# Kernel tuning notes

Measured on AMD Instinct MI355X. Metric: run time of the kernel, lower is better.

## Reference

```python
import jax, jax.numpy as jnp
import numpy as np

B, N_PER, P_PER = 64, 64, 2016   # graphs, nodes/graph, pairs/graph (C(64,2))
IN_DIM, HID, OUT = 64, 128, 10
EDGE_P = 0.125


def _build_graph_structures():
    """Integer preprocessing replicating build_2sets_from_embeddings's
    combinatorics (pairs, iso_type source, triangle-based 2-set edges)."""
    rng = np.random.default_rng(0)
    n, b = N_PER, B
    A = rng.random((b, n, n)) < EDGE_P
    A = np.triu(A, 1)
    A = A | A.transpose(0, 2, 1)                      # symmetric, no self loops
    gs, us, vs = np.nonzero(A)                        # directed edges, both dirs
    edge_index = np.stack([gs * n + us, gs * n + vs]).astype(np.int64)
    batch = np.repeat(np.arange(b), n).astype(np.int64)
    iu, iv = np.triu_indices(n, 1)                    # local pair (u<v) lists
    pidx = np.full((n, n), -1, np.int64)
    pidx[iu, iv] = np.arange(P_PER)
    pidx[iv, iu] = np.arange(P_PER)                   # symmetric lookup = sorted()
    pair_u = (np.arange(b)[:, None] * n + iu[None, :]).ravel().astype(np.int64)
    pair_v = (np.arange(b)[:, None] * n + iv[None, :]).ravel().astype(np.int64)
    iso_type = A[:, iu, iv].astype(np.float32).ravel()[:, None]  # [B*P_PER,1]
    # 2-set edges: pair (u,v) -> sorted(v,w) and sorted(u,w) for every common
    # neighbor w of u and v (matches _build_2set_edges exactly)
    common = A[:, iu, :] & A[:, iv, :]                # (B, P_PER, n)
    g2, ps, ws = np.nonzero(common)
    u, v = iu[ps], iv[ps]
    d1 = pidx[v, ws]
    d2 = pidx[u, ws]
    src = np.concatenate([g2 * P_PER + ps, g2 * P_PER + ps])
    dst = np.concatenate([g2 * P_PER + d1, g2 * P_PER + d2])
    two_edges = np.stack([src, dst]).astype(np.int64)
    two_batch = np.repeat(np.arange(b), P_PER).astype(np.int64)
    return edge_index, batch, pair_u, pair_v, iso_type, two_edges, two_batch


def setup_inputs() -> dict:
    ei, batch, pu, pv, iso, te, tb = _build_graph_structures()
    key = jax.random.key(0)
    ks = jax.random.split(key, 16)
    w = lambda k, i, o: jax.random.normal(k, (i, o), jnp.float32) / np.float32(np.sqrt(i))
    two_in = 2 * HID + 1
    return {
        "x": jax.random.normal(ks[0], (B * N_PER, IN_DIM), jnp.float32),
        "g1_W1_0": w(ks[1], IN_DIM, HID), "g1_W2_0": w(ks[2], IN_DIM, HID),
        "g1_W1_1": w(ks[3], HID, HID),    "g1_W2_1": w(ks[4], HID, HID),
        "g1_W1_2": w(ks[5], HID, HID),    "g1_W2_2": w(ks[6], HID, HID),
        "k_W1_0": w(ks[7], two_in, HID),  "k_W2_0": w(ks[8], two_in, HID),
        "k_W1_1": w(ks[9], HID, HID),     "k_W2_1": w(ks[10], HID, HID),
        "c_W0": w(ks[11], 2 * HID, HID),  "c_b0": jnp.zeros((HID,), jnp.float32),
        "c_W1": w(ks[12], HID, OUT),      "c_b1": jnp.zeros((OUT,), jnp.float32),
        "iso_type": jnp.asarray(iso),
        "edge_index": jnp.asarray(ei), "batch": jnp.asarray(batch),
        "pair_u": jnp.asarray(pu), "pair_v": jnp.asarray(pv),
        "two_edges": jnp.asarray(te), "two_batch": jnp.asarray(tb),
    }


def _mp_layer(h, ei, W1, W2):
    # relu( h @ W1 + scatter_add_{dst}( h[src] @ W2 ) )  -- OneGNNLayer / KSetLayer
    msg = h[ei[0]] @ W2
    agg = jax.ops.segment_sum(msg, ei[1], num_segments=h.shape[0])
    return jax.nn.relu(h @ W1 + agg)


def reference(x, g1_W1_0, g1_W2_0, g1_W1_1, g1_W2_1, g1_W1_2, g1_W2_2,
              k_W1_0, k_W2_0, k_W1_1, k_W2_1,
              c_W0, c_b0, c_W1, c_b1,
              iso_type, edge_index, batch, pair_u, pair_v, two_edges, two_batch):
    h = _mp_layer(x, edge_index, g1_W1_0, g1_W2_0)
    h = _mp_layer(h, edge_index, g1_W1_1, g1_W2_1)
    h = _mp_layer(h, edge_index, g1_W1_2, g1_W2_2)
    graph_emb_1 = jax.ops.segment_sum(h, batch, num_segments=B)
    # 2-set features: [h_u, h_v, iso_type]  -> [P, 2H+1]
    two_x = jnp.concatenate([h[pair_u], h[pair_v], iso_type], axis=1)
    h2 = _mp_layer(two_x, two_edges, k_W1_0, k_W2_0)
    h2 = _mp_layer(h2, two_edges, k_W1_1, k_W2_1)
    graph_emb_2 = jax.ops.segment_sum(h2, two_batch, num_segments=B)
    combined = jnp.concatenate([graph_emb_1, graph_emb_2], axis=1)
    hc = jax.nn.relu(combined @ c_W0 + c_b0)   # Dropout(p=0.5) inactive in eval
    return hc @ c_W1 + c_b1
```

## Files before the change

kernel.cpp:

```cpp
#include <hip/hip_runtime.h>
#include <hip/hip_bf16.h>


typedef short s16x8 __attribute__((ext_vector_type(8)));
typedef float f32x4 __attribute__((ext_vector_type(4)));

__device__ __forceinline__ unsigned short f2bf(float f) {
  union { float f; unsigned u; } x; x.f = f;
  unsigned r = (x.u + 0x7fffu + ((x.u >> 16) & 1u)) >> 16;
  return (unsigned short)r;
}
__device__ __forceinline__ float bf2f(unsigned short h) {
  union { unsigned u; float f; } x; x.u = ((unsigned)h) << 16;
  return x.f;
}
__device__ __forceinline__ float4 ldbf4(const unsigned short* p) {
  ushort4 q = *(const ushort4*)p;
  return make_float4(bf2f(q.x), bf2f(q.y), bf2f(q.z), bf2f(q.w));
}
__device__ __forceinline__ void stbf4(unsigned short* p, float4 v) {
  ushort4 q;
  q.x = f2bf(v.x); q.y = f2bf(v.y); q.z = f2bf(v.z); q.w = f2bf(v.w);
  *(ushort4*)p = q;
}
__device__ __forceinline__ float4 ld4(const float* p) { return *(const float4*)p; }

template<int KCS, int ASTR>
__device__ __forceinline__ void mfma_dual_lds(
    const unsigned short* A, const unsigned short* Wfrag,
    f32x4 (&accA)[8], f32x4 (&accB)[8])
{
  const int lane = threadIdx.x & 63;
  const int wv = threadIdx.x >> 6;
  const int row = wv * 16 + (lane & 15);
  const int k0 = (lane >> 4) << 3;
  const unsigned short* ap = A + row * ASTR + k0;
  const unsigned short* wp = Wfrag + (size_t)lane * 8;
#pragma unroll
  for (int i = 0; i < 8; ++i) { accA[i] = (f32x4)0.f; accB[i] = (f32x4)0.f; }
#pragma unroll
  for (int kc = 0; kc < KCS; ++kc) {
    s16x8 af = *(const s16x8*)(ap + kc * 32);
#pragma unroll
    for (int nt = 0; nt < 8; ++nt) {
      s16x8 b0 = *(const s16x8*)(wp + ((size_t)((nt)*KCS + kc) << 9));
      s16x8 b1 = *(const s16x8*)(wp + ((size_t)((8 + nt) * KCS + kc) << 9));
      accA[nt] = __builtin_amdgcn_mfma_f32_16x16x32_bf16(af, b0, accA[nt], 0, 0, 0);
      accB[nt] = __builtin_amdgcn_mfma_f32_16x16x32_bf16(af, b1, accB[nt], 0, 0, 0);
    }
  }
}

template<int KCS, int ASTR>
__device__ __forceinline__ void mfma_dual_lds16(
    const unsigned short* A, const unsigned short* Wfrag,
    f32x4 (&accA)[2], f32x4 (&accB)[2])
{
  const int lane = threadIdx.x & 63;
  const int w16 = threadIdx.x >> 6;
  const int rw = w16 & 3, ch = w16 >> 2;
  const int row = rw * 16 + (lane & 15);
  const int k0 = (lane >> 4) << 3;
  const unsigned short* ap = A + row * ASTR + k0;
  const unsigned short* wp = Wfrag + (size_t)lane * 8;
  accA[0] = (f32x4)0.f; accA[1] = (f32x4)0.f;
  accB[0] = (f32x4)0.f; accB[1] = (f32x4)0.f;
  __builtin_amdgcn_s_setprio(1);
#pragma unroll
  for (int kc = 0; kc < KCS; ++kc) {
    s16x8 af = *(const s16x8*)(ap + kc * 32);
#pragma unroll
    for (int n2 = 0; n2 < 2; ++n2) {
      int nt = ch * 2 + n2;
      s16x8 b0 = *(const s16x8*)(wp + ((size_t)(nt * KCS + kc) << 9));
      s16x8 b1 = *(const s16x8*)(wp + ((size_t)((8 + nt) * KCS + kc) << 9));
      accA[n2] = __builtin_amdgcn_mfma_f32_16x16x32_bf16(af, b0, accA[n2], 0, 0, 0);
      accB[n2] = __builtin_amdgcn_mfma_f32_16x16x32_bf16(af, b1, accB[n2], 0, 0, 0);
    }
  }
  __builtin_amdgcn_s_setprio(0);
}

__device__ __forceinline__ void epi_lds16(const f32x4 (&accA)[2], const f32x4 (&accB)[2],
    unsigned short (*preS)[136], unsigned short (*msgS)[136])
{
  const int lane = threadIdx.x & 63;
  const int w16 = threadIdx.x >> 6;
  const int rw = w16 & 3, ch = w16 >> 2;
  const int col = lane & 15;
  const int r0 = rw * 16 + ((lane >> 4) << 2);
  __syncthreads();
#pragma unroll
  for (int n2 = 0; n2 < 2; ++n2) {
    int nt = ch * 2 + n2;
#pragma unroll
    for (int r = 0; r < 4; ++r) {
      preS[r0 + r][nt * 16 + col] = f2bf(accA[n2][r]);
      msgS[r0 + r][nt * 16 + col] = f2bf(accB[n2][r]);
    }
  }
  __syncthreads();
}

__device__ __forceinline__ void epi_global(const f32x4 (&accA)[8], const f32x4 (&accB)[8],
    unsigned short (*sOut)[136], unsigned short* Ca, unsigned short* Cb, long tile)
{
  const int tid = threadIdx.x;
  const int lane = tid & 63;
  const int wv = tid >> 6;
  const int col = lane & 15;
  const int r0 = wv * 16 + ((lane >> 4) << 2);
  const long rowBase = tile * 64;
#pragma unroll
  for (int sel = 0; sel < 2; ++sel) {
    __syncthreads();
#pragma unroll
    for (int nt = 0; nt < 8; ++nt) {
#pragma unroll
      for (int r = 0; r < 4; ++r)
        sOut[r0 + r][nt * 16 + col] = f2bf(sel ? accB[nt][r] : accA[nt][r]);
    }
    __syncthreads();
    unsigned short* C = sel ? Cb : Ca;
#pragma unroll
    for (int i = 0; i < 4; ++i) {
      int fi = tid + i * 256;
      int row = fi >> 4;
      int c8 = fi & 15;
      *(uint4*)(C + (rowBase + row) * 128 + c8 * 8) = *(uint4*)&sOut[row][c8 * 8];
    }
  }
}

struct NArgs {
  const float* x;
  const int* ei;
  const int* gstart;
  const unsigned short *Wf0, *Wf1, *Wf2;
  unsigned short* Hn;
  float* ge1;
  int E1;
};

__global__ __launch_bounds__(1024) void node_stage(NArgs a)
{
  __shared__ __align__(16) unsigned short hS[64][136];
  __shared__ __align__(16) unsigned short preS[64][136];
  __shared__ __align__(16) unsigned short msgS[64][136];
  __shared__ int ldeg[64], lcur[64], loff[65];
  __shared__ unsigned short ledge[1024];
  __shared__ float sge[128];

  const int b = blockIdx.x;
  const int t = threadIdx.x;
  const int base = b * 64;

  const int es = a.gstart[b], ee = a.gstart[b + 1];
  if (t < 64) ldeg[t] = 0;
  if (t < 128) sge[t] = 0.f;
  __syncthreads();
  for (int i = es + t; i < ee; i += 1024)
    atomicAdd(&ldeg[a.ei[a.E1 + i] - base], 1);
  __syncthreads();
  if (t < 64) {
    int v = ldeg[t], s = v;
#pragma unroll
    for (int d = 1; d < 64; d <<= 1) {
      int o = __shfl_up(s, d, 64);
      if (t >= d) s += o;
    }
    loff[t] = s - v;
    lcur[t] = s - v;
    if (t == 63) loff[64] = s;
  }
  unsigned short* xs = &preS[0][0];
  for (int i = t; i < 64 * 64; i += 1024) {
    int r = i >> 6, c = i & 63;
    xs[r * 72 + c] = f2bf(a.x[(size_t)(base + r) * 64 + c]);
  }
  __syncthreads();
  for (int i = es + t; i < ee; i += 1024) {
    int s = a.ei[i] - base, d = a.ei[a.E1 + i] - base;
    int pos = atomicAdd(&lcur[d], 1);
    ledge[pos] = (unsigned short)s;
  }
  __syncthreads();

  f32x4 accA[2], accB[2];
  const int grp = t >> 5, f = (t & 31) * 4;

  mfma_dual_lds16<2, 72>(xs, a.Wf0, accA, accB);
  epi_lds16(accA, accB, preS, msgS);
  for (int r = grp; r < 64; r += 32) {
    float4 acc = ldbf4(&preS[r][f]);
    int j1 = loff[r + 1];
    for (int j = loff[r]; j < j1; ++j) {
      float4 m = ldbf4(&msgS[ledge[j]][f]);
      acc.x += m.x; acc.y += m.y; acc.z += m.z; acc.w += m.w;
    }
    stbf4(&hS[r][f], make_float4(fmaxf(acc.x, 0.f), fmaxf(acc.y, 0.f),
                                 fmaxf(acc.z, 0.f), fmaxf(acc.w, 0.f)));
  }
  __syncthreads();

  mfma_dual_lds16<4, 136>(&hS[0][0], a.Wf1, accA, accB);
  epi_lds16(accA, accB, preS, msgS);
  for (int r = grp; r < 64; r += 32) {
    float4 acc = ldbf4(&preS[r][f]);
    int j1 = loff[r + 1];
    for (int j = loff[r]; j < j1; ++j) {
      float4 m = ldbf4(&msgS[ledge[j]][f]);
      acc.x += m.x; acc.y += m.y; acc.z += m.z; acc.w += m.w;
    }
    stbf4(&hS[r][f], make_float4(fmaxf(acc.x, 0.f), fmaxf(acc.y, 0.f),
                                 fmaxf(acc.z, 0.f), fmaxf(acc.w, 0.f)));
  }
  __syncthreads();

  mfma_dual_lds16<4, 136>(&hS[0][0], a.Wf2, accA, accB);
  epi_lds16(accA, accB, preS, msgS);
  {
    float4 g = make_float4(0.f, 0.f, 0.f, 0.f);
    for (int r = grp; r < 64; r += 32) {
      float4 acc = ldbf4(&preS[r][f]);
      int j1 = loff[r + 1];
      for (int j = loff[r]; j < j1; ++j) {
        float4 m = ldbf4(&msgS[ledge[j]][f]);
        acc.x += m.x; acc.y += m.y; acc.z += m.z; acc.w += m.w;
      }
      float4 o = make_float4(fmaxf(acc.x, 0.f), fmaxf(acc.y, 0.f),
                             fmaxf(acc.z, 0.f), fmaxf(acc.w, 0.f));
      stbf4(&hS[r][f], o);
      g.x += o.x; g.y += o.y; g.z += o.z; g.w += o.w;
    }
    atomicAdd(&sge[f + 0], g.x);
    atomicAdd(&sge[f + 1], g.y);
    atomicAdd(&sge[f + 2], g.z);
    atomicAdd(&sge[f + 3], g.w);
  }
  __syncthreads();
  if (t < 128) a.ge1[b * 128 + t] = sge[t];
  {
    int row = t >> 4, c8 = t & 15;
    *(uint4*)(a.Hn + (size_t)(base + row) * 128 + c8 * 8) = *(uint4*)&hS[row][c8 * 8];
  }
}

__global__ __launch_bounds__(256) void hv_gemm(
    const unsigned short* __restrict__ Hn,
    const unsigned short* __restrict__ Wf3, const unsigned short* __restrict__ Wf4,
    unsigned short* __restrict__ HU1, unsigned short* __restrict__ HU2,
    unsigned short* __restrict__ HV1, unsigned short* __restrict__ HV2)
{
  __shared__ __align__(16) unsigned short hS[64][136];
  const int g = blockIdx.x >> 1;
  const int sel = blockIdx.x & 1;
  const int tid = threadIdx.x;
  const unsigned short* src = Hn + (size_t)g * 64 * 128;
#pragma unroll
  for (int i = 0; i < 4; ++i) {
    int fi = tid + i * 256;
    int row = fi >> 4, c8 = fi & 15;
    *(uint4*)&hS[row][c8 * 8] = *(const uint4*)(src + row * 128 + c8 * 8);
  }
  __syncthreads();
  f32x4 accA[8], accB[8];
  mfma_dual_lds<4, 136>(&hS[0][0], sel ? Wf4 : Wf3, accA, accB);
  epi_global(accA, accB, hS, sel ? HV1 : HU1, sel ? HV2 : HU2, g);
}

struct PrepArgs {
  const float* wa[6];
  const float* wb[6];
  unsigned short* Wf[6];
  const int* te; int E2;
  int* degP;
  const int* ei; int E1;
  int* gstart;
  int nCnt;
};

__global__ void prep(PrepArgs p)
{
  int bb = blockIdx.x, t = threadIdx.x;
  if (bb < 88) {
    int gid = bb * 256 + t;
    if (gid < 22528) {
      int pi, local, kcs, kclog;
      if (gid < 2048) { pi = 0; local = gid; kcs = 2; kclog = 1; }
      else { int r = gid - 2048; pi = 1 + (r >> 12); local = r & 4095; kcs = 4; kclog = 2; }
      int lane = local & 63;
      int t1 = local >> 6;
      int kc = t1 & (kcs - 1);
      int t2 = t1 >> kclog;
      int nt = t2 & 7;
      int wsel = t2 >> 3;
      const float* W = wsel ? p.wb[pi] : p.wa[pi];
      int k0 = kc * 32 + ((lane >> 4) << 3);
      int n = nt * 16 + (lane & 15);
      unsigned short tmp[8];
#pragma unroll
      for (int j = 0; j < 8; ++j) tmp[j] = f2bf(W[(size_t)(k0 + j) * 128 + n]);
      *(uint4*)(p.Wf[pi] + (size_t)local * 8) = *(uint4*)tmp;
    }
  } else if (bb < 88 + p.nCnt) {
    int e = (bb - 88) * 256 + t;
    if (e < p.E2) atomicAdd(&p.degP[p.te[p.E2 + e]], 1);
  } else {
    int e = (bb - 88 - p.nCnt) * 256 + t;
    if (e <= p.E1) {
      int ge = (e < p.E1) ? (p.ei[e] >> 6) : 64;
      int gp = (e > 0) ? (p.ei[e - 1] >> 6) : -1;
      for (int g = gp + 1; g <= ge; ++g) p.gstart[g] = e;
    }
  }
}

__global__ __launch_bounds__(256) void scan_reduce(const int* __restrict__ deg,
                                                   int* __restrict__ bsum, int n)
{
  __shared__ int s[256];
  int b = blockIdx.x, t = threadIdx.x;
  int base = b * 1024;
  int v = 0;
#pragma unroll
  for (int i = 0; i < 4; ++i) {
    int idx = base + t + i * 256;
    if (idx < n) v += deg[idx];
  }
  s[t] = v;
  __syncthreads();
  for (int d = 128; d > 0; d >>= 1) {
    if (t < d) s[t] += s[t + d];
    __syncthreads();
  }
  if (t == 0) bsum[b] = s[0];
}

__global__ __launch_bounds__(1024) void scan_partials(int* __restrict__ bsum, int nb)
{
  __shared__ int s[1024];
  int t = threadIdx.x;
  s[t] = (t < nb) ? bsum[t] : 0;
  __syncthreads();
  for (int d = 1; d < 1024; d <<= 1) {
    int v = (t >= d) ? s[t - d] : 0;
    __syncthreads();
    s[t] += v;
    __syncthreads();
  }
  if (t < nb) bsum[t] = (t == 0) ? 0 : s[t - 1];
  if (t == 1023) bsum[nb] = s[1023];
}

__global__ __launch_bounds__(256) void scan_final(const int* __restrict__ deg,
                                                  const int* __restrict__ bsum,
                                                  int* __restrict__ off,
                                                  int* __restrict__ cur, int n, int nb)
{
  __shared__ int s[256];
  int b = blockIdx.x, t = threadIdx.x;
  int base = b * 1024 + t * 4;
  int v0 = 0, v1 = 0, v2 = 0, v3 = 0;
  if (base + 0 < n) v0 = deg[base + 0];
  if (base + 1 < n) v1 = deg[base + 1];
  if (base + 2 < n) v2 = deg[base + 2];
  if (base + 3 < n) v3 = deg[base + 3];
  s[t] = v0 + v1 + v2 + v3;
  __syncthreads();
  for (int d = 1; d < 256; d <<= 1) {
    int v = (t >= d) ? s[t - d] : 0;
    __syncthreads();
    s[t] += v;
    __syncthreads();
  }
  int run = bsum[b] + ((t == 0) ? 0 : s[t - 1]);
  if (base + 0 < n) { off[base + 0] = run; cur[base + 0] = run; run += v0; }
  if (base + 1 < n) { off[base + 1] = run; cur[base + 1] = run; run += v1; }
  if (base + 2 < n) { off[base + 2] = run; cur[base + 2] = run; run += v2; }
  if (base + 3 < n) { off[base + 3] = run; cur[base + 3] = run; run += v3; }
  if (b == 0 && t == 0) off[n] = bsum[nb];
}

__global__ void csr_fill_pair(const int* __restrict__ te, int E2,
                              const int* __restrict__ pu, const int* __restrict__ pv,
                              const float* __restrict__ iso,
                              int* __restrict__ curP, int4* __restrict__ recP)
{
  int e = blockIdx.x * 256 + threadIdx.x;
  if (e >= E2) return;
  int s = te[e], d = te[E2 + e];
  int pos = atomicAdd(&curP[d], 1);
  recP[pos] = make_int4(pu[s], pv[s], __float_as_int(iso[s]), s);
}

__global__ __launch_bounds__(256) void gather_two0_t(
    const unsigned short* __restrict__ HU1, const unsigned short* __restrict__ HV1,
    const unsigned short* __restrict__ HU2, const unsigned short* __restrict__ HV2,
    const float* __restrict__ iso,
    const float* __restrict__ w1iso, const float* __restrict__ w2iso,
    const int* __restrict__ pu, const int* __restrict__ pv,
    const int* __restrict__ off, const int4* __restrict__ rec,
    unsigned short* __restrict__ out)
{
  __shared__ int offS[65];
  __shared__ int puS[64], pvS[64];
  __shared__ float isoS[64];
  __shared__ __align__(16) int4 recS[512];

  const int tid = threadIdx.x;
  int tile = (int)blockIdx.x;
  const int nT = (int)gridDim.x;
  if ((nT & 7) == 0)
    tile = (tile & 7) * (nT >> 3) + (tile >> 3);
  const int p0 = tile * 64;

  if (tid < 65) offS[tid] = off[p0 + tid];
  if (tid < 64) { puS[tid] = pu[p0 + tid]; pvS[tid] = pv[p0 + tid]; isoS[tid] = iso[p0 + tid]; }
  __syncthreads();
  const int e0 = offS[0];
  const int ecnt = offS[64] - e0;
  const bool useS = (ecnt <= 512);
  if (useS)
    for (int j = tid; j < ecnt; j += 256) recS[j] = rec[e0 + j];
  __syncthreads();

  const int grp = tid >> 5;
  const int f = (tid & 31) * 4;
  const float4 wi1 = ld4(w1iso + f);
  const float4 wi2 = ld4(w2iso + f);
  for (int pi = grp; pi < 64; pi += 8) {
    float4 a = ldbf4(HU1 + (size_t)puS[pi] * 128 + f);
    float4 b = ldbf4(HV1 + (size_t)pvS[pi] * 128 + f);
    float is0 = isoS[pi];
    float4 acc;
    acc.x = a.x + b.x + is0 * wi1.x;
    acc.y = a.y + b.y + is0 * wi1.y;
    acc.z = a.z + b.z + is0 * wi1.z;
    acc.w = a.w + b.w + is0 * wi1.w;
    int j = offS[pi], e1 = offS[pi + 1];
    for (; j + 1 < e1; j += 2) {
      int4 r0 = useS ? recS[j - e0] : rec[j];
      int4 r1 = useS ? recS[j + 1 - e0] : rec[j + 1];
      float4 mu0 = ldbf4(HU2 + (size_t)r0.x * 128 + f);
      float4 mv0 = ldbf4(HV2 + (size_t)r0.y * 128 + f);
      float4 mu1 = ldbf4(HU2 + (size_t)r1.x * 128 + f);
      float4 mv1 = ldbf4(HV2 + (size_t)r1.y * 128 + f);
      float i0 = __int_as_float(r0.z), i1 = __int_as_float(r1.z);
      acc.x += mu0.x + mv0.x + i0 * wi2.x + mu1.x + mv1.x + i1 * wi2.x;
      acc.y += mu0.y + mv0.y + i0 * wi2.y + mu1.y + mv1.y + i1 * wi2.y;
      acc.z += mu0.z + mv0.z + i0 * wi2.z + mu1.z + mv1.z + i1 * wi2.z;
      acc.w += mu0.w + mv0.w + i0 * wi2.w + mu1.w + mv1.w + i1 * wi2.w;
    }
    if (j < e1) {
      int4 r0 = useS ? recS[j - e0] : rec[j];
      float4 mu0 = ldbf4(HU2 + (size_t)r0.x * 128 + f);
      float4 mv0 = ldbf4(HV2 + (size_t)r0.y * 128 + f);
      float i0 = __int_as_float(r0.z);
      acc.x += mu0.x + mv0.x + i0 * wi2.x;
      acc.y += mu0.y + mv0.y + i0 * wi2.y;
      acc.z += mu0.z + mv0.z + i0 * wi2.z;
      acc.w += mu0.w + mv0.w + i0 * wi2.w;
    }
    stbf4(out + (size_t)(p0 + pi) * 128 + f,
          make_float4(fmaxf(acc.x, 0.f), fmaxf(acc.y, 0.f),
                      fmaxf(acc.z, 0.f), fmaxf(acc.w, 0.f)));
  }
}

__global__ __launch_bounds__(256) void pair_l1(
    const unsigned short* __restrict__ H2,
    const unsigned short* __restrict__ Wfrag,
    const int* __restrict__ off, const int4* __restrict__ rec,
    float* __restrict__ gep)
{
  __shared__ __align__(16) unsigned short aggS[64][136];
  __shared__ int offS[65];
  __shared__ int recwS[768];
  __shared__ float sge[256];

  const int tid = threadIdx.x;
  int tile = (int)blockIdx.x;
  const int nT = (int)gridDim.x;
  if ((nT & 7) == 0)
    tile = (tile & 7) * (nT >> 3) + (tile >> 3);
  const int r0 = tile * 64;

  if (tid < 65) offS[tid] = off[r0 + tid];
  sge[tid] = 0.f;

  const int lane = tid & 63;
  const int wv = tid >> 6;
  const int arow = wv * 16 + (lane & 15);
  const int k0 = (lane >> 4) << 3;
  const unsigned short* hrow = H2 + (size_t)(r0 + arow) * 128 + k0;
  s16x8 ah[4];
#pragma unroll
  for (int kc = 0; kc < 4; ++kc) ah[kc] = *(const s16x8*)(hrow + kc * 32);

  __syncthreads();
  const int e0 = offS[0];
  const int ecnt = offS[64] - e0;
  const bool useS = (ecnt <= 768);
  if (useS)
    for (int j = tid; j < ecnt; j += 256) recwS[j] = rec[e0 + j].w;
  __syncthreads();

  {
    const int grp = tid >> 5, f = (tid & 31) * 4;
    for (int i = grp; i < 64; i += 8) {
      float4 acc = make_float4(0.f, 0.f, 0.f, 0.f);
      int j = offS[i], e1 = offS[i + 1];
      for (; j + 1 < e1; j += 2) {
        int s0 = useS ? recwS[j - e0] : rec[j].w;
        int s1 = useS ? recwS[j + 1 - e0] : rec[j + 1].w;
        float4 m0 = ldbf4(H2 + (size_t)s0 * 128 + f);
        float4 m1 = ldbf4(H2 + (size_t)s1 * 128 + f);
        acc.x += m0.x + m1.x; acc.y += m0.y + m1.y;
        acc.z += m0.z + m1.z; acc.w += m0.w + m1.w;
      }
      if (j < e1) {
        int s0 = useS ? recwS[j - e0] : rec[j].w;
        float4 m0 = ldbf4(H2 + (size_t)s0 * 128 + f);
        acc.x += m0.x; acc.y += m0.y; acc.z += m0.z; acc.w += m0.w;
      }
      stbf4(&aggS[i][f], acc);
    }
  }
  __syncthreads();

  const unsigned short* gp = &aggS[0][0] + arow * 136 + k0;
  const unsigned short* wp = Wfrag + (size_t)lane * 8;
  f32x4 acc[8];
#pragma unroll
  for (int nt = 0; nt < 8; ++nt) acc[nt] = (f32x4)0.f;
  __builtin_amdgcn_s_setprio(1);
#pragma unroll
  for (int kc = 0; kc < 4; ++kc) {
    s16x8 ag = *(const s16x8*)(gp + kc * 32);
#pragma unroll
    for (int nt = 0; nt < 8; ++nt) {
      s16x8 b0 = *(const s16x8*)(wp + ((size_t)(nt * 4 + kc) << 9));
      s16x8 b1 = *(const s16x8*)(wp + ((size_t)((8 + nt) * 4 + kc) << 9));
      acc[nt] = __builtin_amdgcn_mfma_f32_16x16x32_bf16(ah[kc], b0, acc[nt], 0, 0, 0);
      acc[nt] = __builtin_amdgcn_mfma_f32_16x16x32_bf16(ag, b1, acc[nt], 0, 0, 0);
    }
  }
  __builtin_amdgcn_s_setprio(0);

  const int half = wv >> 1;
  const int col0 = lane & 15;
#pragma unroll
  for (int nt = 0; nt < 8; ++nt) {
    float s = fmaxf(acc[nt][0], 0.f) + fmaxf(acc[nt][1], 0.f)
            + fmaxf(acc[nt][2], 0.f) + fmaxf(acc[nt][3], 0.f);
    atomicAdd(&sge[half * 128 + nt * 16 + col0], s);
  }
  __syncthreads();
  gep[(size_t)tile * 256 + tid] = sge[tid];
}

__global__ void classifier(const float* __restrict__ ge1, const float* __restrict__ gep,
                           const float* __restrict__ W0, const float* __restrict__ b0,
                           const float* __restrict__ W1, const float* __restrict__ b1,
                           float* __restrict__ out)
{
  __shared__ float comb[256];
  __shared__ float hc[128];
  int g = blockIdx.x, t = threadIdx.x;
  comb[t] = ge1[g * 128 + t];
  float s2 = 0.f;
  const float* gpr = gep + (size_t)g * 63 * 128 + t;
  for (int i = 0; i < 63; ++i) s2 += gpr[i * 128];
  comb[t + 128] = s2;
  __syncthreads();
  float s = b0[t];
  for (int k = 0; k < 256; ++k) s += comb[k] * W0[k * 128 + t];
  hc[t] = fmaxf(s, 0.f);
  __syncthreads();
  if (t < 10) {
    float s2o = b1[t];
    for (int k = 0; k < 128; ++k) s2o += hc[k] * W1[k * 10 + t];
    out[g * 10 + t] = s2o;
  }
}

extern "C" void kernel_launch(void* const* d_in, const int* in_sizes, int n_in,
                              void* d_out, int out_size, void* d_ws, size_t ws_size,
                              hipStream_t stream)
{
  (void)n_in; (void)out_size; (void)ws_size;
  const float* x       = (const float*)d_in[0];
  const float* g1_W1_0 = (const float*)d_in[1];
  const float* g1_W2_0 = (const float*)d_in[2];
  const float* g1_W1_1 = (const float*)d_in[3];
  const float* g1_W2_1 = (const float*)d_in[4];
  const float* g1_W1_2 = (const float*)d_in[5];
  const float* g1_W2_2 = (const float*)d_in[6];
  const float* k_W1_0  = (const float*)d_in[7];
  const float* k_W2_0  = (const float*)d_in[8];
  const float* k_W1_1  = (const float*)d_in[9];
  const float* k_W2_1  = (const float*)d_in[10];
  const float* c_W0    = (const float*)d_in[11];
  const float* c_b0    = (const float*)d_in[12];
  const float* c_W1    = (const float*)d_in[13];
  const float* c_b1    = (const float*)d_in[14];
  const float* iso     = (const float*)d_in[15];
  const int*   ei      = (const int*)d_in[16];
  const int*   pu      = (const int*)d_in[18];
  const int*   pv      = (const int*)d_in[19];
  const int*   te      = (const int*)d_in[20];

  const int N  = in_sizes[0] / 64;
  const int E1 = in_sizes[16] / 2;
  const int P  = in_sizes[18];
  const int E2 = in_sizes[20] / 2;
  const int B  = 64;
  const int nTiles = P / 64;

  const size_t NH = (size_t)N * 128;
  const size_t PH = (size_t)P * 128;

  float* ge1 = (float*)d_ws;
  float* gep = ge1 + 8192;
  unsigned short* HU1 = (unsigned short*)(gep + (size_t)2 * nTiles * 128);
  unsigned short* HV1 = HU1 + NH;
  unsigned short* HU2 = HV1 + NH;
  unsigned short* HV2 = HU2 + NH;
  unsigned short* H2   = HV2 + NH;
  unsigned short* Hn   = H2 + PH;
  unsigned short* Wf0  = Hn + NH;
  unsigned short* Wf1  = Wf0 + 16384;
  unsigned short* Wf2  = Wf1 + 32768;
  unsigned short* Wf3  = Wf2 + 32768;
  unsigned short* Wf4  = Wf3 + 32768;
  unsigned short* Wf5  = Wf4 + 32768;

  size_t ipOff = ((size_t)((char*)(Wf5 + 32768) - (char*)d_ws) + 15) & ~(size_t)15;
  int4* recP   = (int4*)((char*)d_ws + ipOff);
  int* degP    = (int*)(recP + E2);
  int* offP    = degP + P;
  int* curP    = offP + P + 1;
  int* bsumP   = curP + P;
  int* gstartN = bsumP + 128;

  const int nbP  = (P + 1023) / 1024;
  const int nCnt = (E2 + 255) / 256;
  const int nBnd = (E1 + 256) / 256;

  hipMemsetAsync(degP, 0, (size_t)P * 4, stream);

  PrepArgs pa;
  pa.wa[0] = g1_W1_0;           pa.wb[0] = g1_W2_0;
  pa.wa[1] = g1_W1_1;           pa.wb[1] = g1_W2_1;
  pa.wa[2] = g1_W1_2;           pa.wb[2] = g1_W2_2;
  pa.wa[3] = k_W1_0;            pa.wb[3] = k_W2_0;
  pa.wa[4] = k_W1_0 + 128*128;  pa.wb[4] = k_W2_0 + 128*128;
  pa.wa[5] = k_W1_1;            pa.wb[5] = k_W2_1;
  pa.Wf[0] = Wf0; pa.Wf[1] = Wf1; pa.Wf[2] = Wf2;
  pa.Wf[3] = Wf3; pa.Wf[4] = Wf4; pa.Wf[5] = Wf5;
  pa.te = te; pa.E2 = E2; pa.degP = degP;
  pa.ei = ei; pa.E1 = E1; pa.gstart = gstartN; pa.nCnt = nCnt;
  prep<<<88 + nCnt + nBnd, 256, 0, stream>>>(pa);

  scan_reduce<<<nbP, 256, 0, stream>>>(degP, bsumP, P);
  scan_partials<<<1, 1024, 0, stream>>>(bsumP, nbP);
  scan_final<<<nbP, 256, 0, stream>>>(degP, bsumP, offP, curP, P, nbP);
  csr_fill_pair<<<nCnt, 256, 0, stream>>>(te, E2, pu, pv, iso, curP, recP);

  NArgs na;
  na.x = x; na.ei = ei; na.gstart = gstartN; na.E1 = E1;
  na.Wf0 = Wf0; na.Wf1 = Wf1; na.Wf2 = Wf2;
  na.Hn = Hn; na.ge1 = ge1;
  node_stage<<<B, 1024, 0, stream>>>(na);

  hv_gemm<<<2 * B, 256, 0, stream>>>(Hn, Wf3, Wf4, HU1, HU2, HV1, HV2);

  gather_two0_t<<<nTiles, 256, 0, stream>>>(HU1, HV1, HU2, HV2, iso,
                                            k_W1_0 + 256 * 128, k_W2_0 + 256 * 128,
                                            pu, pv, offP, recP, H2);

  pair_l1<<<nTiles, 256, 0, stream>>>(H2, Wf5, offP, recP, gep);

  classifier<<<B, 128, 0, stream>>>(ge1, gep, c_W0, c_b0, c_W1, c_b1, (float*)d_out);
}
```

Before: 302.4 us.

## Fuse pair layer-0 gather into pair layer-1 by recomputing neighbor features

Merges the two pair-level kernels into one. Each tile builds its own layer-0 features in shared memory, and it recomputes every neighbor pair's layer-0 row on the fly from the HU/HV tables instead of reading a materialized H2 buffer. This removes the global H2 write and read and one kernel launch. In exchange it adds two-hop gather work proportional to neighbor degree, and the larger shared-memory footprint may lower occupancy.

```diff
diff --git a/kernel.cpp b/kernel.cpp
--- a/kernel.cpp
+++ b/kernel.cpp
@@ -394,19 +394,24 @@
   recP[pos] = make_int4(pu[s], pv[s], __float_as_int(iso[s]), s);
 }
 
-__global__ __launch_bounds__(256) void gather_two0_t(
+__global__ __launch_bounds__(256) void pair_fused(
     const unsigned short* __restrict__ HU1, const unsigned short* __restrict__ HV1,
     const unsigned short* __restrict__ HU2, const unsigned short* __restrict__ HV2,
     const float* __restrict__ iso,
     const float* __restrict__ w1iso, const float* __restrict__ w2iso,
     const int* __restrict__ pu, const int* __restrict__ pv,
     const int* __restrict__ off, const int4* __restrict__ rec,
-    unsigned short* __restrict__ out)
-{
+    const unsigned short* __restrict__ Wfrag,
+    float* __restrict__ gep)
+{
+  __shared__ __align__(16) unsigned short hS[64][136];
+  __shared__ __align__(16) unsigned short aggS[64][136];
   __shared__ int offS[65];
   __shared__ int puS[64], pvS[64];
   __shared__ float isoS[64];
   __shared__ __align__(16) int4 recS[512];
+  __shared__ int so0S[512], so1S[512];
+  __shared__ float sge[256];
 
   const int tid = threadIdx.x;
   int tile = (int)blockIdx.x;
@@ -417,119 +422,92 @@
 
   if (tid < 65) offS[tid] = off[p0 + tid];
   if (tid < 64) { puS[tid] = pu[p0 + tid]; pvS[tid] = pv[p0 + tid]; isoS[tid] = iso[p0 + tid]; }
+  sge[tid] = 0.f;
   __syncthreads();
   const int e0 = offS[0];
   const int ecnt = offS[64] - e0;
   const bool useS = (ecnt <= 512);
-  if (useS)
+  if (useS) {
     for (int j = tid; j < ecnt; j += 256) recS[j] = rec[e0 + j];
+    __syncthreads();
+    for (int j = tid; j < ecnt; j += 256) {
+      int s = recS[j].w;
+      so0S[j] = off[s];
+      so1S[j] = off[s + 1];
+    }
+  }
   __syncthreads();
 
   const int grp = tid >> 5;
   const int f = (tid & 31) * 4;
   const float4 wi1 = ld4(w1iso + f);
   const float4 wi2 = ld4(w2iso + f);
-  for (int pi = grp; pi < 64; pi += 8) {
-    float4 a = ldbf4(HU1 + (size_t)puS[pi] * 128 + f);
-    float4 b = ldbf4(HV1 + (size_t)pvS[pi] * 128 + f);
-    float is0 = isoS[pi];
-    float4 acc;
-    acc.x = a.x + b.x + is0 * wi1.x;
-    acc.y = a.y + b.y + is0 * wi1.y;
-    acc.z = a.z + b.z + is0 * wi1.z;
-    acc.w = a.w + b.w + is0 * wi1.w;
-    int j = offS[pi], e1 = offS[pi + 1];
-    for (; j + 1 < e1; j += 2) {
-      int4 r0 = useS ? recS[j - e0] : rec[j];
-      int4 r1 = useS ? recS[j + 1 - e0] : rec[j + 1];
-      float4 mu0 = ldbf4(HU2 + (size_t)r0.x * 128 + f);
-      float4 mv0 = ldbf4(HV2 + (size_t)r0.y * 128 + f);
-      float4 mu1 = ldbf4(HU2 + (size_t)r1.x * 128 + f);
-      float4 mv1 = ldbf4(HV2 + (size_t)r1.y * 128 + f);
-      float i0 = __int_as_float(r0.z), i1 = __int_as_float(r1.z);
-      acc.x += mu0.x + mv0.x + i0 * wi2.x + mu1.x + mv1.x + i1 * wi2.x;
-      acc.y += mu0.y + mv0.y + i0 * wi2.y + mu1.y + mv1.y + i1 * wi2.y;
-      acc.z += mu0.z + mv0.z + i0 * wi2.z + mu1.z + mv1.z + i1 * wi2.z;
-      acc.w += mu0.w + mv0.w + i0 * wi2.w + mu1.w + mv1.w + i1 * wi2.w;
-    }
-    if (j < e1) {
-      int4 r0 = useS ? recS[j - e0] : rec[j];
-      float4 mu0 = ldbf4(HU2 + (size_t)r0.x * 128 + f);
-      float4 mv0 = ldbf4(HV2 + (size_t)r0.y * 128 + f);
-      float i0 = __int_as_float(r0.z);
-      acc.x += mu0.x + mv0.x + i0 * wi2.x;
-      acc.y += mu0.y + mv0.y + i0 * wi2.y;
-      acc.z += mu0.z + mv0.z + i0 * wi2.z;
-      acc.w += mu0.w + mv0.w + i0 * wi2.w;
-    }
-    stbf4(out + (size_t)(p0 + pi) * 128 + f,
-          make_float4(fmaxf(acc.x, 0.f), fmaxf(acc.y, 0.f),
-                      fmaxf(acc.z, 0.f), fmaxf(acc.w, 0.f)));
-  }
-}
-
-__global__ __launch_bounds__(256) void pair_l1(
-    const unsigned short* __restrict__ H2,
-    const unsigned short* __restrict__ Wfrag,
-    const int* __restrict__ off, const int4* __restrict__ rec,
-    float* __restrict__ gep)
-{
-  __shared__ __align__(16) unsigned short aggS[64][136];
-  __shared__ int offS[65];
-  __shared__ int recwS[768];
-  __shared__ float sge[256];
-
-  const int tid = threadIdx.x;
-  int tile = (int)blockIdx.x;
-  const int nT = (int)gridDim.x;
-  if ((nT & 7) == 0)
-    tile = (tile & 7) * (nT >> 3) + (tile >> 3);
-  const int r0 = tile * 64;
-
-  if (tid < 65) offS[tid] = off[r0 + tid];
-  sge[tid] = 0.f;
+
+  for (int i = grp; i < 64; i += 8) {
+    float4 a = ldbf4(HU1 + (size_t)puS[i] * 128 + f);
+    float4 b = ldbf4(HV1 + (size_t)pvS[i] * 128 + f);
+    float is0 = isoS[i];
+    float4 t;
+    t.x = a.x + b.x + is0 * wi1.x;
+    t.y = a.y + b.y + is0 * wi1.y;
+    t.z = a.z + b.z + is0 * wi1.z;
+    t.w = a.w + b.w + is0 * wi1.w;
+    int j = offS[i], e1 = offS[i + 1];
+    for (; j < e1; ++j) {
+      int4 r = useS ? recS[j - e0] : rec[j];
+      float4 mu = ldbf4(HU2 + (size_t)r.x * 128 + f);
+      float4 mv = ldbf4(HV2 + (size_t)r.y * 128 + f);
+      float i0 = __int_as_float(r.z);
+      t.x += mu.x + mv.x + i0 * wi2.x;
+      t.y += mu.y + mv.y + i0 * wi2.y;
+      t.z += mu.z + mv.z + i0 * wi2.z;
+      t.w += mu.w + mv.w + i0 * wi2.w;
+    }
+    stbf4(&hS[i][f], make_float4(fmaxf(t.x, 0.f), fmaxf(t.y, 0.f),
+                                 fmaxf(t.z, 0.f), fmaxf(t.w, 0.f)));
+  }
+
+  for (int i = grp; i < 64; i += 8) {
+    float4 agg = make_float4(0.f, 0.f, 0.f, 0.f);
+    int j = offS[i], e1 = offS[i + 1];
+    for (; j < e1; ++j) {
+      int jl = j - e0;
+      int4 r; int ks, ke;
+      if (useS) { r = recS[jl]; ks = so0S[jl]; ke = so1S[jl]; }
+      else { r = rec[j]; int s = r.w; ks = off[s]; ke = off[s + 1]; }
+      float4 a = ldbf4(HU1 + (size_t)r.x * 128 + f);
+      float4 b = ldbf4(HV1 + (size_t)r.y * 128 + f);
+      float i0 = __int_as_float(r.z);
+      float4 t;
+      t.x = a.x + b.x + i0 * wi1.x;
+      t.y = a.y + b.y + i0 * wi1.y;
+      t.z = a.z + b.z + i0 * wi1.z;
+      t.w = a.w + b.w + i0 * wi1.w;
+      for (int k = ks; k < ke; ++k) {
+        int4 q = rec[k];
+        float4 mu = ldbf4(HU2 + (size_t)q.x * 128 + f);
+        float4 mv = ldbf4(HV2 + (size_t)q.y * 128 + f);
+        float qi = __int_as_float(q.z);
+        t.x += mu.x + mv.x + qi * wi2.x;
+        t.y += mu.y + mv.y + qi * wi2.y;
+        t.z += mu.z + mv.z + qi * wi2.z;
+        t.w += mu.w + mv.w + qi * wi2.w;
+      }
+      agg.x += fmaxf(t.x, 0.f);
+      agg.y += fmaxf(t.y, 0.f);
+      agg.z += fmaxf(t.z, 0.f);
+      agg.w += fmaxf(t.w, 0.f);
+    }
+    stbf4(&aggS[i][f], agg);
+  }
+  __syncthreads();
 
   const int lane = tid & 63;
   const int wv = tid >> 6;
   const int arow = wv * 16 + (lane & 15);
   const int k0 = (lane >> 4) << 3;
-  const unsigned short* hrow = H2 + (size_t)(r0 + arow) * 128 + k0;
-  s16x8 ah[4];
-#pragma unroll
-  for (int kc = 0; kc < 4; ++kc) ah[kc] = *(const s16x8*)(hrow + kc * 32);
-
-  __syncthreads();
-  const int e0 = offS[0];
-  const int ecnt = offS[64] - e0;
-  const bool useS = (ecnt <= 768);
-  if (useS)
-    for (int j = tid; j < ecnt; j += 256) recwS[j] = rec[e0 + j].w;
-  __syncthreads();
-
-  {
-    const int grp = tid >> 5, f = (tid & 31) * 4;
-    for (int i = grp; i < 64; i += 8) {
-      float4 acc = make_float4(0.f, 0.f, 0.f, 0.f);
-      int j = offS[i], e1 = offS[i + 1];
-      for (; j + 1 < e1; j += 2) {
-        int s0 = useS ? recwS[j - e0] : rec[j].w;
-        int s1 = useS ? recwS[j + 1 - e0] : rec[j + 1].w;
-        float4 m0 = ldbf4(H2 + (size_t)s0 * 128 + f);
-        float4 m1 = ldbf4(H2 + (size_t)s1 * 128 + f);
-        acc.x += m0.x + m1.x; acc.y += m0.y + m1.y;
-        acc.z += m0.z + m1.z; acc.w += m0.w + m1.w;
-      }
-      if (j < e1) {
-        int s0 = useS ? recwS[j - e0] : rec[j].w;
-        float4 m0 = ldbf4(H2 + (size_t)s0 * 128 + f);
-        acc.x += m0.x; acc.y += m0.y; acc.z += m0.z; acc.w += m0.w;
-      }
-      stbf4(&aggS[i][f], acc);
-    }
-  }
-  __syncthreads();
-
-  const unsigned short* gp = &aggS[0][0] + arow * 136 + k0;
+  const unsigned short* hp = &hS[0][0] + arow * 136 + k0;
+  const unsigned short* gpp = &aggS[0][0] + arow * 136 + k0;
   const unsigned short* wp = Wfrag + (size_t)lane * 8;
   f32x4 acc[8];
 #pragma unroll
@@ -537,12 +515,13 @@
   __builtin_amdgcn_s_setprio(1);
 #pragma unroll
   for (int kc = 0; kc < 4; ++kc) {
-    s16x8 ag = *(const s16x8*)(gp + kc * 32);
+    s16x8 ah = *(const s16x8*)(hp + kc * 32);
+    s16x8 ag = *(const s16x8*)(gpp + kc * 32);
 #pragma unroll
     for (int nt = 0; nt < 8; ++nt) {
       s16x8 b0 = *(const s16x8*)(wp + ((size_t)(nt * 4 + kc) << 9));
       s16x8 b1 = *(const s16x8*)(wp + ((size_t)((8 + nt) * 4 + kc) << 9));
-      acc[nt] = __builtin_amdgcn_mfma_f32_16x16x32_bf16(ah[kc], b0, acc[nt], 0, 0, 0);
+      acc[nt] = __builtin_amdgcn_mfma_f32_16x16x32_bf16(ah, b0, acc[nt], 0, 0, 0);
       acc[nt] = __builtin_amdgcn_mfma_f32_16x16x32_bf16(ag, b1, acc[nt], 0, 0, 0);
     }
   }
@@ -619,7 +598,6 @@
   const int nTiles = P / 64;
 
   const size_t NH = (size_t)N * 128;
-  const size_t PH = (size_t)P * 128;
 
   float* ge1 = (float*)d_ws;
   float* gep = ge1 + 8192;
@@ -627,8 +605,7 @@
   unsigned short* HV1 = HU1 + NH;
   unsigned short* HU2 = HV1 + NH;
   unsigned short* HV2 = HU2 + NH;
-  unsigned short* H2   = HV2 + NH;
-  unsigned short* Hn   = H2 + PH;
+  unsigned short* Hn   = HV2 + NH;
   unsigned short* Wf0  = Hn + NH;
   unsigned short* Wf1  = Wf0 + 16384;
   unsigned short* Wf2  = Wf1 + 32768;
@@ -676,11 +653,9 @@
 
   hv_gemm<<<2 * B, 256, 0, stream>>>(Hn, Wf3, Wf4, HU1, HU2, HV1, HV2);
 
-  gather_two0_t<<<nTiles, 256, 0, stream>>>(HU1, HV1, HU2, HV2, iso,
-                                            k_W1_0 + 256 * 128, k_W2_0 + 256 * 128,
-                                            pu, pv, offP, recP, H2);
-
-  pair_l1<<<nTiles, 256, 0, stream>>>(H2, Wf5, offP, recP, gep);
+  pair_fused<<<nTiles, 256, 0, stream>>>(HU1, HV1, HU2, HV2, iso,
+                                         k_W1_0 + 256 * 128, k_W2_0 + 256 * 128,
+                                         pu, pv, offP, recP, Wf5, gep);
 
   classifier<<<B, 128, 0, stream>>>(ge1, gep, c_W0, c_b0, c_W1, c_b1, (float*)d_out);
 }
```

Result: slower. 499.3 us (+65.1%).
